# Optimization experiments

Measured on AMD Instinct MI355X. Metric: run time of the kernel, lower is better.

Reference implementation:

```python
import jax, jax.numpy as jnp
import numpy as np

EPS = 10.0
MAX_ITER = 50
THRESH = 1e-05
N, M, D = 8192, 8192, 32


def setup_inputs() -> dict:
    key = jax.random.key(0)
    k1, k2, k3, k4 = jax.random.split(key, 4)
    x = jax.random.normal(k1, (N, D), dtype=jnp.float32)
    y = jax.random.normal(k2, (M, D), dtype=jnp.float32)
    p = jax.random.uniform(k3, (N,), dtype=jnp.float32)
    q = jax.random.uniform(k4, (M,), dtype=jnp.float32)
    p = p / jnp.sum(p)  # marginals must be probability vectors
    q = q / jnp.sum(q)
    return {"x": x, "y": y, "p": p, "q": q}


def _cost_matrix_l2(x, y):
    # ||x_i - y_j||^2 via the expansion, avoiding the [N, M, D] intermediate
    x2 = jnp.sum(x * x, axis=-1)  # [N]
    y2 = jnp.sum(y * y, axis=-1)  # [M]
    C = x2[:, None] + y2[None, :] - 2.0 * (x @ y.T)  # [N, M]
    return jnp.maximum(C, 0.0)


def reference(x, y, p, q):
    C = _cost_matrix_l2(x, y)          # [N, M]
    K = jnp.exp(-C / EPS)              # [N, M]

    def step(carry, _):
        a, b, done = carry
        a_new = p / (K @ b)            # [N]
        b_new = q / (K.T @ a_new)      # [M]
        err = jnp.linalg.norm(b_new - b)
        # emulate the early break: freeze (a, b) once err < thresh was hit
        a_out = jnp.where(done, a, a_new)
        b_out = jnp.where(done, b, b_new)
        done = jnp.logical_or(done, err < THRESH)
        return (a_out, b_out, done), None

    init = (jnp.zeros_like(p), jnp.ones_like(q), jnp.array(False))
    (a, b, _), _ = jax.lax.scan(step, init, None, length=MAX_ITER)

    T = a[:, None] * K * b[None, :]    # diag(a) @ K @ diag(b)
    w_cost = jnp.sum(T * C)
    return w_cost, T
```

## Files before the change

kernel.cpp:

```cpp
#include <hip/hip_runtime.h>
#include <hip/hip_fp16.h>


#define NN 8192
#define DDIM 32
#define EPSF 10.0f
#define LOG2E 1.44269504088896340736f
#define LN2F 0.69314718055994530942f
#define KLOG2 8.0f
#define THRESH2 1e-10f

#define OFF_KS   0ull
#define OFF_PART (67108864ull)
#define OFF_A    (OFF_PART + 8388608ull)
#define OFF_B    (OFF_A + 32768ull)
#define OFF_X2   (OFF_B + 32768ull)
#define OFF_Y2   (OFF_X2 + 32768ull)
#define OFF_ERR  (OFF_Y2 + 32768ull)
#define WS_NEEDED (OFF_ERR + 4096ull)

typedef float floatx2 __attribute__((ext_vector_type(2)));

#if __has_builtin(__builtin_amdgcn_cvt_pk_f32_fp8) && __has_builtin(__builtin_amdgcn_cvt_pk_fp8_f32)
#define HW_FP8 1
#else
#define HW_FP8 0
#include <hip/hip_fp8.h>
#endif

__device__ __forceinline__ void fp8x4_to_f32(unsigned int w, float* f) {
#if HW_FP8
    floatx2 lo = __builtin_amdgcn_cvt_pk_f32_fp8((int)w, false);
    floatx2 hi = __builtin_amdgcn_cvt_pk_f32_fp8((int)w, true);
    f[0] = lo.x; f[1] = lo.y; f[2] = hi.x; f[3] = hi.y;
#else
    for (int i = 0; i < 4; ++i) {
        __hip_fp8_e4m3 h; h.__x = (__hip_fp8_storage_t)((w >> (8 * i)) & 0xff);
        f[i] = (float)h;
    }
#endif
}

__device__ __forceinline__ unsigned char f32_to_fp8(float v) {
#if HW_FP8
    return (unsigned char)(__builtin_amdgcn_cvt_pk_fp8_f32(v, v, 0, false) & 0xff);
#else
    __hip_fp8_e4m3 h(v);
    return (unsigned char)h.__x;
#endif
}

__global__ __launch_bounds__(256) void k_init(const float* __restrict__ x,
                                              const float* __restrict__ y,
                                              float* __restrict__ x2,
                                              float* __restrict__ y2,
                                              float* __restrict__ b,
                                              float* __restrict__ err,
                                              float* __restrict__ out) {
    int t = blockIdx.x * 256 + threadIdx.x;
    const float4* x4 = (const float4*)(x + (size_t)t * DDIM);
    float s = 0.f;
#pragma unroll
    for (int k = 0; k < 8; ++k) { float4 v = x4[k]; s += v.x*v.x + v.y*v.y + v.z*v.z + v.w*v.w; }
    x2[t] = s;
    const float4* y4 = (const float4*)(y + (size_t)t * DDIM);
    s = 0.f;
#pragma unroll
    for (int k = 0; k < 8; ++k) { float4 v = y4[k]; s += v.x*v.x + v.y*v.y + v.z*v.z + v.w*v.w; }
    y2[t] = s;
    b[t] = 1.0f;
    if (t < 2) err[t] = 1e30f;
    if (t == 0) out[0] = 0.f;
}

__global__ __launch_bounds__(256) void k_build(const float* __restrict__ x,
                                               const float* __restrict__ y,
                                               const float* __restrict__ x2,
                                               const float* __restrict__ y2,
                                               unsigned char* __restrict__ Ks) {
    __shared__ float yT[DDIM][256];
    __shared__ float xT[DDIM][32];
    __shared__ __align__(16) unsigned char hb8[32][256];
    const int t = threadIdx.x;
    const int jb = blockIdx.x & 31;
    const int ib = blockIdx.x >> 5;
    const int colbase = jb * 256, rowbase = ib * 32;

    {
        const float4* yp = (const float4*)(y + (size_t)(colbase + t) * DDIM);
#pragma unroll
        for (int k = 0; k < 8; ++k) {
            float4 v = yp[k];
            yT[4*k+0][t] = v.x; yT[4*k+1][t] = v.y; yT[4*k+2][t] = v.z; yT[4*k+3][t] = v.w;
        }
    }
    {
        int r = t >> 3, ds = (t & 7) * 4;
        float4 v = *(const float4*)(x + (size_t)(rowbase + r) * DDIM + ds);
        xT[ds+0][r] = v.x; xT[ds+1][r] = v.y; xT[ds+2][r] = v.z; xT[ds+3][r] = v.w;
    }
    __syncthreads();

    float acc[32];
#pragma unroll
    for (int r = 0; r < 32; ++r) acc[r] = 0.f;
    for (int d = 0; d < DDIM; ++d) {
        float yv = yT[d][t];
#pragma unroll
        for (int r4 = 0; r4 < 8; ++r4) {
            float4 xv = *(const float4*)&xT[d][r4 * 4];
            acc[r4*4+0] = fmaf(xv.x, yv, acc[r4*4+0]);
            acc[r4*4+1] = fmaf(xv.y, yv, acc[r4*4+1]);
            acc[r4*4+2] = fmaf(xv.z, yv, acc[r4*4+2]);
            acc[r4*4+3] = fmaf(xv.w, yv, acc[r4*4+3]);
        }
    }
    const float y2c = y2[colbase + t];
#pragma unroll
    for (int r = 0; r < 32; ++r) {
        float Cv = fmaxf(x2[rowbase + r] + y2c - 2.f * acc[r], 0.f);
        float arg = KLOG2 - Cv * (LOG2E / EPSF);
        hb8[r][t] = f32_to_fp8(__builtin_amdgcn_exp2f(arg));
    }
    __syncthreads();
    {
        int row = t >> 3, off = (t & 7) * 32;
        uint4 v0 = *(const uint4*)&hb8[row][off];
        uint4 v1 = *(const uint4*)&hb8[row][off + 16];
        unsigned char* dst = Ks + (size_t)(rowbase + row) * NN + colbase + off;
        *(uint4*)dst = v0;
        *(uint4*)(dst + 16) = v1;
    }
}

#if HW_FP8
#define ROWFMA(KV, KC) { \
    const unsigned int* kw_ = (const unsigned int*)&(KV); \
    _Pragma("unroll") \
    for (int j4 = 0; j4 < 4; ++j4) { \
        floatx2 lo_ = __builtin_amdgcn_cvt_pk_f32_fp8((int)kw_[j4], false); \
        floatx2 hi_ = __builtin_amdgcn_cvt_pk_f32_fp8((int)kw_[j4], true); \
        const floatx2* bp_ = (const floatx2*)(b4 + ((KC) * 4 + j4) * 64 + lane); \
        rs2a += lo_ * bp_[0]; \
        rs2b += hi_ * bp_[1]; \
    } }
#define COLFMA(KV, AV) { \
    floatx2 av2_; av2_.x = (AV); av2_.y = (AV); \
    floatx2 l0_ = __builtin_amdgcn_cvt_pk_f32_fp8((int)(KV).x, false); \
    floatx2 h0_ = __builtin_amdgcn_cvt_pk_f32_fp8((int)(KV).x, true); \
    floatx2 l1_ = __builtin_amdgcn_cvt_pk_f32_fp8((int)(KV).y, false); \
    floatx2 h1_ = __builtin_amdgcn_cvt_pk_f32_fp8((int)(KV).y, true); \
    cacc2[0] += l0_ * av2_; cacc2[1] += h0_ * av2_; \
    cacc2[2] += l1_ * av2_; cacc2[3] += h1_ * av2_; }
#else
#define ROWFMA(KV, KC) { \
    const unsigned int* kw_ = (const unsigned int*)&(KV); \
    _Pragma("unroll") \
    for (int j4 = 0; j4 < 4; ++j4) { \
        float kf_[4]; \
        fp8x4_to_f32(kw_[j4], kf_); \
        float4 bv_ = b4[((KC) * 4 + j4) * 64 + lane]; \
        rs2a.x = fmaf(kf_[0], bv_.x, rs2a.x); \
        rs2b.x = fmaf(kf_[1], bv_.y, rs2b.x); \
        rs2a.y = fmaf(kf_[2], bv_.z, rs2a.y); \
        rs2b.y = fmaf(kf_[3], bv_.w, rs2b.y); \
    } }
#define COLFMA(KV, AV) { \
    float kf_[8]; \
    fp8x4_to_f32((KV).x, kf_); \
    fp8x4_to_f32((KV).y, kf_ + 4); \
    cacc2[0].x = fmaf(kf_[0], (AV), cacc2[0].x); \
    cacc2[0].y = fmaf(kf_[1], (AV), cacc2[0].y); \
    cacc2[1].x = fmaf(kf_[2], (AV), cacc2[1].x); \
    cacc2[1].y = fmaf(kf_[3], (AV), cacc2[1].y); \
    cacc2[2].x = fmaf(kf_[4], (AV), cacc2[2].x); \
    cacc2[2].y = fmaf(kf_[5], (AV), cacc2[2].y); \
    cacc2[3].x = fmaf(kf_[6], (AV), cacc2[3].x); \
    cacc2[3].y = fmaf(kf_[7], (AV), cacc2[3].y); }
#endif

__global__ __launch_bounds__(1024) void k_iter(const unsigned char* __restrict__ Ks,
                                               const float* __restrict__ bg,
                                               const float* __restrict__ p,
                                               float* __restrict__ a_out,
                                               float* __restrict__ part,
                                               float* __restrict__ err, int it) {
    __shared__ float bsw[NN];
    __shared__ float rowhalf[2][8][2];
    const int t = threadIdx.x;
    const int w = t >> 6, lane = t & 63;
    const int band = blockIdx.x * 32;
    const int rl = w >> 1, half = w & 1;

    float4 g0 = ((const float4*)bg)[2 * t];
    float4 g1 = ((const float4*)bg)[2 * t + 1];
    const uint4* kp0 = (const uint4*)(Ks + (size_t)(band + rl) * NN + half * 4096);
    uint4 ka0 = kp0[lane], ka1 = kp0[64 + lane], ka2 = kp0[128 + lane], ka3 = kp0[192 + lane];
    float ev = err[(it ^ 1) & 1];
    if (blockIdx.x == 0 && t == 0) err[it & 1] = 0.f;
    __builtin_amdgcn_sched_barrier(0);
    if (ev < THRESH2) return;

    {
        float vals[8] = {g0.x, g0.y, g0.z, g0.w, g1.x, g1.y, g1.z, g1.w};
        int c0 = t * 8;
#pragma unroll
        for (int u = 0; u < 8; ++u) {
            int c = c0 + u;
            bsw[(c >> 10) * 1024 + ((c >> 2) & 3) * 256 + ((c >> 4) & 63) * 4 + (c & 3)] = vals[u];
        }
    }
    __syncthreads();

    floatx2 cacc2[4];
    cacc2[0] = floatx2{0.f, 0.f}; cacc2[1] = floatx2{0.f, 0.f};
    cacc2[2] = floatx2{0.f, 0.f}; cacc2[3] = floatx2{0.f, 0.f};
    const float4* b4 = (const float4*)bsw;

#pragma unroll
    for (int sub = 0; sub < 4; ++sub) {
        const int sb = sub & 1;
        const uint2* kp2 = (const uint2*)(Ks + (size_t)(band + sub * 8) * NN);
        uint2 cv0 = kp2[0 * (NN / 8) + t], cv1 = kp2[1 * (NN / 8) + t],
              cv2 = kp2[2 * (NN / 8) + t], cv3 = kp2[3 * (NN / 8) + t],
              cv4 = kp2[4 * (NN / 8) + t], cv5 = kp2[5 * (NN / 8) + t],
              cv6 = kp2[6 * (NN / 8) + t], cv7 = kp2[7 * (NN / 8) + t];
        uint4 kb0 = {0,0,0,0}, kb1 = {0,0,0,0}, kb2 = {0,0,0,0}, kb3 = {0,0,0,0};
        if (sub < 3) {
            const uint4* kp = (const uint4*)(Ks + (size_t)(band + (sub + 1) * 8 + rl) * NN + half * 4096);
            kb0 = kp[lane]; kb1 = kp[64 + lane]; kb2 = kp[128 + lane]; kb3 = kp[192 + lane];
        }
        __builtin_amdgcn_sched_barrier(0);

        floatx2 rs2a = floatx2{0.f, 0.f}, rs2b = floatx2{0.f, 0.f};
        ROWFMA(ka0, half * 4 + 0)
        ROWFMA(ka1, half * 4 + 1)
        ROWFMA(ka2, half * 4 + 2)
        ROWFMA(ka3, half * 4 + 3)
        float rs = (rs2a.x + rs2a.y) + (rs2b.x + rs2b.y);
#pragma unroll
        for (int off = 32; off > 0; off >>= 1) rs += __shfl_down(rs, off, 64);
        if (lane == 0) rowhalf[sb][rl][half] = rs;
        __syncthreads();

        const int rg = band + sub * 8;
        float av0 = p[rg + 0] * __builtin_amdgcn_rcpf(rowhalf[sb][0][0] + rowhalf[sb][0][1]);
        float av1 = p[rg + 1] * __builtin_amdgcn_rcpf(rowhalf[sb][1][0] + rowhalf[sb][1][1]);
        float av2 = p[rg + 2] * __builtin_amdgcn_rcpf(rowhalf[sb][2][0] + rowhalf[sb][2][1]);
        float av3 = p[rg + 3] * __builtin_amdgcn_rcpf(rowhalf[sb][3][0] + rowhalf[sb][3][1]);
        float av4 = p[rg + 4] * __builtin_amdgcn_rcpf(rowhalf[sb][4][0] + rowhalf[sb][4][1]);
        float av5 = p[rg + 5] * __builtin_amdgcn_rcpf(rowhalf[sb][5][0] + rowhalf[sb][5][1]);
        float av6 = p[rg + 6] * __builtin_amdgcn_rcpf(rowhalf[sb][6][0] + rowhalf[sb][6][1]);
        float av7 = p[rg + 7] * __builtin_amdgcn_rcpf(rowhalf[sb][7][0] + rowhalf[sb][7][1]);
        if (t == 0) {
            *(float4*)(a_out + rg)     = make_float4(av0, av1, av2, av3);
            *(float4*)(a_out + rg + 4) = make_float4(av4, av5, av6, av7);
        }

        COLFMA(cv0, av0)
        COLFMA(cv1, av1)
        COLFMA(cv2, av2)
        COLFMA(cv3, av3)
        COLFMA(cv4, av4)
        COLFMA(cv5, av5)
        COLFMA(cv6, av6)
        COLFMA(cv7, av7)

        if (sub < 3) { ka0 = kb0; ka1 = kb1; ka2 = kb2; ka3 = kb3; }
    }
    float4* pp = (float4*)(part + (size_t)blockIdx.x * NN + t * 8);
    pp[0] = make_float4(cacc2[0].x, cacc2[0].y, cacc2[1].x, cacc2[1].y);
    pp[1] = make_float4(cacc2[2].x, cacc2[2].y, cacc2[3].x, cacc2[3].y);
}

__global__ __launch_bounds__(256) void k_div(const float* __restrict__ part,
                                             const float* __restrict__ q,
                                             float* __restrict__ b,
                                             float* __restrict__ err, int it) {
    if (err[(it ^ 1) & 1] < THRESH2) return;
    const int t = threadIdx.x;
    const int c = t & 31, ibc = t >> 5;
    const int col = blockIdx.x * 32 + c;
    float s = 0.f;
#pragma unroll 4
    for (int i = 0; i < 32; ++i) s += part[(size_t)(ibc * 32 + i) * NN + col];
    __shared__ float red[8][32];
    __shared__ float esc[32];
    red[ibc][c] = s;
    __syncthreads();
    if (ibc == 0) {
        float sum = 0.f;
#pragma unroll
        for (int k = 0; k < 8; ++k) sum += red[k][c];
        float bn = q[col] / sum;
        float d = bn - b[col];
        b[col] = bn;
        esc[c] = d * d;
    }
    __syncthreads();
    if (t == 0) {
        float e = 0.f;
#pragma unroll
        for (int k = 0; k < 32; ++k) e += esc[k];
        atomicAdd(&err[it & 1], e);
    }
}

__global__ __launch_bounds__(256) void k_final(const unsigned char* __restrict__ Ks,
                                               const float* __restrict__ a,
                                               const float* __restrict__ b,
                                               float* __restrict__ out) {
    const int t = threadIdx.x;
    const int row = blockIdx.x;
    const float ai = a[row];
    const uint2* kp = (const uint2*)(Ks + (size_t)row * NN);
    float* Trow = out + 1 + (size_t)row * NN;
    float w = 0.f;
    const float c1 = EPSF * LN2F;
#pragma unroll
    for (int k = 0; k < 4; ++k) {
        const int col = k * 2048 + t * 8;
        uint2 kv = kp[k * 256 + t];
        float kf[8];
        fp8x4_to_f32(kv.x, kf);
        fp8x4_to_f32(kv.y, kf + 4);
        float4 b0 = *(const float4*)(b + col);
        float4 b1 = *(const float4*)(b + col + 4);
        float bv[8] = {b0.x, b0.y, b0.z, b0.w, b1.x, b1.y, b1.z, b1.w};
#pragma unroll
        for (int j = 0; j < 8; ++j) {
            float ks = kf[j];
            float Tv = ai * ks * bv[j];
            float Cv = c1 * (KLOG2 - __builtin_amdgcn_logf(fmaxf(ks, 1e-35f)));
            w = fmaf(Tv, Cv, w);
            Trow[col + j] = Tv;
        }
    }
#pragma unroll
    for (int off = 32; off > 0; off >>= 1) w += __shfl_down(w, off, 64);
    __shared__ float red[4];
    if ((t & 63) == 0) red[t >> 6] = w;
    __syncthreads();
    if (t == 0) atomicAdd(out, (red[0] + red[1]) + (red[2] + red[3]));
}

extern "C" void kernel_launch(void* const* d_in, const int* in_sizes, int n_in,
                              void* d_out, int out_size, void* d_ws, size_t ws_size,
                              hipStream_t stream) {
    const float* x = (const float*)d_in[0];
    const float* y = (const float*)d_in[1];
    const float* p = (const float*)d_in[2];
    const float* q = (const float*)d_in[3];
    float* out = (float*)d_out;
    if (ws_size < WS_NEEDED) return;
    char* ws = (char*)d_ws;
    unsigned char* Ks = (unsigned char*)(ws + OFF_KS);
    float* part = (float*)(ws + OFF_PART);
    float* a = (float*)(ws + OFF_A);
    float* b = (float*)(ws + OFF_B);
    float* x2 = (float*)(ws + OFF_X2);
    float* y2 = (float*)(ws + OFF_Y2);
    float* err = (float*)(ws + OFF_ERR);

    k_init<<<dim3(32), dim3(256), 0, stream>>>(x, y, x2, y2, b, err, out);
    k_build<<<dim3(8192), dim3(256), 0, stream>>>(x, y, x2, y2, Ks);
    for (int it = 0; it < 50; ++it) {
        k_iter<<<dim3(256), dim3(1024), 0, stream>>>(Ks, b, p, a, part, err, it);
        k_div<<<dim3(256), dim3(256), 0, stream>>>(part, q, b, err, it);
    }
    k_final<<<dim3(8192), dim3(256), 0, stream>>>(Ks, a, b, out);
}
```

Measured before the change: 1.792 ms.

## Fuse Sinkhorn iterations into one cooperative persistent kernel with grid barriers

```diff
diff --git a/kernel.cpp b/kernel.cpp
--- a/kernel.cpp
+++ b/kernel.cpp
@@ -9,6 +9,7 @@
 #define LN2F 0.69314718055994530942f
 #define KLOG2 8.0f
 #define THRESH2 1e-10f
+#define GRIDN 256
 
 #define OFF_KS   0ull
 #define OFF_PART (67108864ull)
@@ -17,6 +18,7 @@
 #define OFF_X2   (OFF_B + 32768ull)
 #define OFF_Y2   (OFF_X2 + 32768ull)
 #define OFF_ERR  (OFF_Y2 + 32768ull)
+#define OFF_BAR  (OFF_ERR + 256ull)
 #define WS_NEEDED (OFF_ERR + 4096ull)
 
 typedef float floatx2 __attribute__((ext_vector_type(2)));
@@ -50,12 +52,32 @@
 #endif
 }
 
+__device__ __forceinline__ void gsync(int* bar) {
+    __syncthreads();
+    if (threadIdx.x == 0) {
+        __threadfence();
+        int g = __hip_atomic_load(bar + 1, __ATOMIC_RELAXED, __HIP_MEMORY_SCOPE_AGENT);
+        if (__hip_atomic_fetch_add(bar, 1, __ATOMIC_ACQ_REL, __HIP_MEMORY_SCOPE_AGENT) == GRIDN - 1) {
+            __hip_atomic_store(bar, 0, __ATOMIC_RELAXED, __HIP_MEMORY_SCOPE_AGENT);
+            __hip_atomic_store(bar + 1, g + 1, __ATOMIC_RELEASE, __HIP_MEMORY_SCOPE_AGENT);
+        } else {
+            int guard = 1 << 20;
+            while (__hip_atomic_load(bar + 1, __ATOMIC_RELAXED, __HIP_MEMORY_SCOPE_AGENT) == g
+                   && --guard)
+                __builtin_amdgcn_s_sleep(2);
+        }
+        __threadfence();
+    }
+    __syncthreads();
+}
+
 __global__ __launch_bounds__(256) void k_init(const float* __restrict__ x,
                                               const float* __restrict__ y,
                                               float* __restrict__ x2,
                                               float* __restrict__ y2,
                                               float* __restrict__ b,
                                               float* __restrict__ err,
+                                              int* __restrict__ bar,
                                               float* __restrict__ out) {
     int t = blockIdx.x * 256 + threadIdx.x;
     const float4* x4 = (const float4*)(x + (size_t)t * DDIM);
@@ -69,7 +91,7 @@
     for (int k = 0; k < 8; ++k) { float4 v = y4[k]; s += v.x*v.x + v.y*v.y + v.z*v.z + v.w*v.w; }
     y2[t] = s;
     b[t] = 1.0f;
-    if (t < 2) err[t] = 1e30f;
+    if (t < 2) { err[t] = 1e30f; bar[t] = 0; }
     if (t == 0) out[0] = 0.f;
 }
 
@@ -179,6 +201,149 @@
     cacc2[3].y = fmaf(kf_[7], (AV), cacc2[3].y); }
 #endif
 
+__device__ __forceinline__ void phaseA(const unsigned char* __restrict__ Ks,
+                                       const float* __restrict__ bg,
+                                       const float* __restrict__ p,
+                                       float* __restrict__ a_out,
+                                       float* __restrict__ part,
+                                       float* bsw, float (*rowhalf)[8][2],
+                                       int t, int w, int lane, int band,
+                                       int rl, int half) {
+    float4 g0 = ((const float4*)bg)[2 * t];
+    float4 g1 = ((const float4*)bg)[2 * t + 1];
+    const uint4* kp0 = (const uint4*)(Ks + (size_t)(band + rl) * NN + half * 4096);
+    uint4 ka0 = kp0[lane], ka1 = kp0[64 + lane], ka2 = kp0[128 + lane], ka3 = kp0[192 + lane];
+    __builtin_amdgcn_sched_barrier(0);
+    {
+        float vals[8] = {g0.x, g0.y, g0.z, g0.w, g1.x, g1.y, g1.z, g1.w};
+        int c0 = t * 8;
+#pragma unroll
+        for (int u = 0; u < 8; ++u) {
+            int c = c0 + u;
+            bsw[(c >> 10) * 1024 + ((c >> 2) & 3) * 256 + ((c >> 4) & 63) * 4 + (c & 3)] = vals[u];
+        }
+    }
+    __syncthreads();
+
+    floatx2 cacc2[4];
+    cacc2[0] = floatx2{0.f, 0.f}; cacc2[1] = floatx2{0.f, 0.f};
+    cacc2[2] = floatx2{0.f, 0.f}; cacc2[3] = floatx2{0.f, 0.f};
+    const float4* b4 = (const float4*)bsw;
+
+#pragma unroll
+    for (int sub = 0; sub < 4; ++sub) {
+        const int sb = sub & 1;
+        const uint2* kp2 = (const uint2*)(Ks + (size_t)(band + sub * 8) * NN);
+        uint2 cv0 = kp2[0 * (NN / 8) + t], cv1 = kp2[1 * (NN / 8) + t],
+              cv2 = kp2[2 * (NN / 8) + t], cv3 = kp2[3 * (NN / 8) + t],
+              cv4 = kp2[4 * (NN / 8) + t], cv5 = kp2[5 * (NN / 8) + t],
+              cv6 = kp2[6 * (NN / 8) + t], cv7 = kp2[7 * (NN / 8) + t];
+        uint4 kb0 = {0,0,0,0}, kb1 = {0,0,0,0}, kb2 = {0,0,0,0}, kb3 = {0,0,0,0};
+        if (sub < 3) {
+            const uint4* kp = (const uint4*)(Ks + (size_t)(band + (sub + 1) * 8 + rl) * NN + half * 4096);
+            kb0 = kp[lane]; kb1 = kp[64 + lane]; kb2 = kp[128 + lane]; kb3 = kp[192 + lane];
+        }
+        __builtin_amdgcn_sched_barrier(0);
+
+        floatx2 rs2a = floatx2{0.f, 0.f}, rs2b = floatx2{0.f, 0.f};
+        ROWFMA(ka0, half * 4 + 0)
+        ROWFMA(ka1, half * 4 + 1)
+        ROWFMA(ka2, half * 4 + 2)
+        ROWFMA(ka3, half * 4 + 3)
+        float rs = (rs2a.x + rs2a.y) + (rs2b.x + rs2b.y);
+#pragma unroll
+        for (int off = 32; off > 0; off >>= 1) rs += __shfl_down(rs, off, 64);
+        if (lane == 0) rowhalf[sb][rl][half] = rs;
+        __syncthreads();
+
+        const int rg = band + sub * 8;
+        float av0 = p[rg + 0] * __builtin_amdgcn_rcpf(rowhalf[sb][0][0] + rowhalf[sb][0][1]);
+        float av1 = p[rg + 1] * __builtin_amdgcn_rcpf(rowhalf[sb][1][0] + rowhalf[sb][1][1]);
+        float av2 = p[rg + 2] * __builtin_amdgcn_rcpf(rowhalf[sb][2][0] + rowhalf[sb][2][1]);
+        float av3 = p[rg + 3] * __builtin_amdgcn_rcpf(rowhalf[sb][3][0] + rowhalf[sb][3][1]);
+        float av4 = p[rg + 4] * __builtin_amdgcn_rcpf(rowhalf[sb][4][0] + rowhalf[sb][4][1]);
+        float av5 = p[rg + 5] * __builtin_amdgcn_rcpf(rowhalf[sb][5][0] + rowhalf[sb][5][1]);
+        float av6 = p[rg + 6] * __builtin_amdgcn_rcpf(rowhalf[sb][6][0] + rowhalf[sb][6][1]);
+        float av7 = p[rg + 7] * __builtin_amdgcn_rcpf(rowhalf[sb][7][0] + rowhalf[sb][7][1]);
+        if (t == 0) {
+            *(float4*)(a_out + rg)     = make_float4(av0, av1, av2, av3);
+            *(float4*)(a_out + rg + 4) = make_float4(av4, av5, av6, av7);
+        }
+
+        COLFMA(cv0, av0)
+        COLFMA(cv1, av1)
+        COLFMA(cv2, av2)
+        COLFMA(cv3, av3)
+        COLFMA(cv4, av4)
+        COLFMA(cv5, av5)
+        COLFMA(cv6, av6)
+        COLFMA(cv7, av7)
+
+        if (sub < 3) { ka0 = kb0; ka1 = kb1; ka2 = kb2; ka3 = kb3; }
+    }
+    float4* pp = (float4*)(part + (size_t)blockIdx.x * NN + t * 8);
+    pp[0] = make_float4(cacc2[0].x, cacc2[0].y, cacc2[1].x, cacc2[1].y);
+    pp[1] = make_float4(cacc2[2].x, cacc2[2].y, cacc2[3].x, cacc2[3].y);
+}
+
+__global__ __launch_bounds__(1024) void k_loop(const unsigned char* __restrict__ Ks,
+                                               float* __restrict__ bg,
+                                               const float* __restrict__ p,
+                                               const float* __restrict__ q,
+                                               float* __restrict__ a_out,
+                                               float* __restrict__ part,
+                                               float* __restrict__ err,
+                                               int* __restrict__ bar) {
+    __shared__ float bsw[NN];
+    __shared__ float rowhalf[2][8][2];
+    __shared__ float redB[32][32];
+    __shared__ float esc[32];
+    const int t = threadIdx.x;
+    const int w = t >> 6, lane = t & 63;
+    const int band = blockIdx.x * 32;
+    const int rl = w >> 1, half = w & 1;
+    const int cB = t & 31, ibcB = t >> 5;
+    const int colB = blockIdx.x * 32 + cB;
+
+    for (int it = 0; it < 50; ++it) {
+        float ev = __hip_atomic_load(&err[(it ^ 1) & 1], __ATOMIC_RELAXED, __HIP_MEMORY_SCOPE_AGENT);
+        if (ev < THRESH2) break;
+        if (blockIdx.x == 0 && t == 0)
+            __hip_atomic_store(&err[it & 1], 0.f, __ATOMIC_RELAXED, __HIP_MEMORY_SCOPE_AGENT);
+
+        phaseA(Ks, bg, p, a_out, part, bsw, rowhalf, t, w, lane, band, rl, half);
+
+        gsync(bar);
+
+        {
+            float s = 0.f;
+#pragma unroll
+            for (int i = 0; i < 8; ++i) s += part[(size_t)(ibcB * 8 + i) * NN + colB];
+            redB[ibcB][cB] = s;
+            __syncthreads();
+            if (t < 32) {
+                float sum = 0.f;
+#pragma unroll
+                for (int k2 = 0; k2 < 32; ++k2) sum += redB[k2][t];
+                const int col = blockIdx.x * 32 + t;
+                float bn = q[col] / sum;
+                float d = bn - bg[col];
+                bg[col] = bn;
+                esc[t] = d * d;
+            }
+            __syncthreads();
+            if (t == 0) {
+                float e = 0.f;
+#pragma unroll
+                for (int k2 = 0; k2 < 32; ++k2) e += esc[k2];
+                atomicAdd(&err[it & 1], e);
+            }
+        }
+
+        gsync(bar);
+    }
+}
+
 __global__ __launch_bounds__(1024) void k_iter(const unsigned char* __restrict__ Ks,
                                                const float* __restrict__ bg,
                                                const float* __restrict__ p,
@@ -191,86 +356,10 @@
     const int w = t >> 6, lane = t & 63;
     const int band = blockIdx.x * 32;
     const int rl = w >> 1, half = w & 1;
-
-    float4 g0 = ((const float4*)bg)[2 * t];
-    float4 g1 = ((const float4*)bg)[2 * t + 1];
-    const uint4* kp0 = (const uint4*)(Ks + (size_t)(band + rl) * NN + half * 4096);
-    uint4 ka0 = kp0[lane], ka1 = kp0[64 + lane], ka2 = kp0[128 + lane], ka3 = kp0[192 + lane];
     float ev = err[(it ^ 1) & 1];
     if (blockIdx.x == 0 && t == 0) err[it & 1] = 0.f;
-    __builtin_amdgcn_sched_barrier(0);
     if (ev < THRESH2) return;
-
-    {
-        float vals[8] = {g0.x, g0.y, g0.z, g0.w, g1.x, g1.y, g1.z, g1.w};
-        int c0 = t * 8;
-#pragma unroll
-        for (int u = 0; u < 8; ++u) {
-            int c = c0 + u;
-            bsw[(c >> 10) * 1024 + ((c >> 2) & 3) * 256 + ((c >> 4) & 63) * 4 + (c & 3)] = vals[u];
-        }
-    }
-    __syncthreads();
-
-    floatx2 cacc2[4];
-    cacc2[0] = floatx2{0.f, 0.f}; cacc2[1] = floatx2{0.f, 0.f};
-    cacc2[2] = floatx2{0.f, 0.f}; cacc2[3] = floatx2{0.f, 0.f};
-    const float4* b4 = (const float4*)bsw;
-
-#pragma unroll
-    for (int sub = 0; sub < 4; ++sub) {
-        const int sb = sub & 1;
-        const uint2* kp2 = (const uint2*)(Ks + (size_t)(band + sub * 8) * NN);
-        uint2 cv0 = kp2[0 * (NN / 8) + t], cv1 = kp2[1 * (NN / 8) + t],
-              cv2 = kp2[2 * (NN / 8) + t], cv3 = kp2[3 * (NN / 8) + t],
-              cv4 = kp2[4 * (NN / 8) + t], cv5 = kp2[5 * (NN / 8) + t],
-              cv6 = kp2[6 * (NN / 8) + t], cv7 = kp2[7 * (NN / 8) + t];
-        uint4 kb0 = {0,0,0,0}, kb1 = {0,0,0,0}, kb2 = {0,0,0,0}, kb3 = {0,0,0,0};
-        if (sub < 3) {
-            const uint4* kp = (const uint4*)(Ks + (size_t)(band + (sub + 1) * 8 + rl) * NN + half * 4096);
-            kb0 = kp[lane]; kb1 = kp[64 + lane]; kb2 = kp[128 + lane]; kb3 = kp[192 + lane];
-        }
-        __builtin_amdgcn_sched_barrier(0);
-
-        floatx2 rs2a = floatx2{0.f, 0.f}, rs2b = floatx2{0.f, 0.f};
-        ROWFMA(ka0, half * 4 + 0)
-        ROWFMA(ka1, half * 4 + 1)
-        ROWFMA(ka2, half * 4 + 2)
-        ROWFMA(ka3, half * 4 + 3)
-        float rs = (rs2a.x + rs2a.y) + (rs2b.x + rs2b.y);
-#pragma unroll
-        for (int off = 32; off > 0; off >>= 1) rs += __shfl_down(rs, off, 64);
-        if (lane == 0) rowhalf[sb][rl][half] = rs;
-        __syncthreads();
-
-        const int rg = band + sub * 8;
-        float av0 = p[rg + 0] * __builtin_amdgcn_rcpf(rowhalf[sb][0][0] + rowhalf[sb][0][1]);
-        float av1 = p[rg + 1] * __builtin_amdgcn_rcpf(rowhalf[sb][1][0] + rowhalf[sb][1][1]);
-        float av2 = p[rg + 2] * __builtin_amdgcn_rcpf(rowhalf[sb][2][0] + rowhalf[sb][2][1]);
-        float av3 = p[rg + 3] * __builtin_amdgcn_rcpf(rowhalf[sb][3][0] + rowhalf[sb][3][1]);
-        float av4 = p[rg + 4] * __builtin_amdgcn_rcpf(rowhalf[sb][4][0] + rowhalf[sb][4][1]);
-        float av5 = p[rg + 5] * __builtin_amdgcn_rcpf(rowhalf[sb][5][0] + rowhalf[sb][5][1]);
-        float av6 = p[rg + 6] * __builtin_amdgcn_rcpf(rowhalf[sb][6][0] + rowhalf[sb][6][1]);
-        float av7 = p[rg + 7] * __builtin_amdgcn_rcpf(rowhalf[sb][7][0] + rowhalf[sb][7][1]);
-        if (t == 0) {
-            *(float4*)(a_out + rg)     = make_float4(av0, av1, av2, av3);
-            *(float4*)(a_out + rg + 4) = make_float4(av4, av5, av6, av7);
-        }
-
-        COLFMA(cv0, av0)
-        COLFMA(cv1, av1)
-        COLFMA(cv2, av2)
-        COLFMA(cv3, av3)
-        COLFMA(cv4, av4)
-        COLFMA(cv5, av5)
-        COLFMA(cv6, av6)
-        COLFMA(cv7, av7)
-
-        if (sub < 3) { ka0 = kb0; ka1 = kb1; ka2 = kb2; ka3 = kb3; }
-    }
-    float4* pp = (float4*)(part + (size_t)blockIdx.x * NN + t * 8);
-    pp[0] = make_float4(cacc2[0].x, cacc2[0].y, cacc2[1].x, cacc2[1].y);
-    pp[1] = make_float4(cacc2[2].x, cacc2[2].y, cacc2[3].x, cacc2[3].y);
+    phaseA(Ks, bg, p, a_out, part, bsw, rowhalf, t, w, lane, band, rl, half);
 }
 
 __global__ __launch_bounds__(256) void k_div(const float* __restrict__ part,
@@ -361,12 +450,21 @@
     float* x2 = (float*)(ws + OFF_X2);
     float* y2 = (float*)(ws + OFF_Y2);
     float* err = (float*)(ws + OFF_ERR);
-
-    k_init<<<dim3(32), dim3(256), 0, stream>>>(x, y, x2, y2, b, err, out);
+    int* bar = (int*)(ws + OFF_BAR);
+
+    k_init<<<dim3(32), dim3(256), 0, stream>>>(x, y, x2, y2, b, err, bar, out);
     k_build<<<dim3(8192), dim3(256), 0, stream>>>(x, y, x2, y2, Ks);
-    for (int it = 0; it < 50; ++it) {
-        k_iter<<<dim3(256), dim3(1024), 0, stream>>>(Ks, b, p, a, part, err, it);
-        k_div<<<dim3(256), dim3(256), 0, stream>>>(part, q, b, err, it);
+
+    void* args[] = { (void*)&Ks, (void*)&b, (void*)&p, (void*)&q,
+                     (void*)&a, (void*)&part, (void*)&err, (void*)&bar };
+    hipError_t ce = hipLaunchCooperativeKernel((void*)k_loop, dim3(GRIDN), dim3(1024),
+                                               args, 0, stream);
+    if (ce != hipSuccess) {
+        (void)hipGetLastError();
+        for (int it = 0; it < 50; ++it) {
+            k_iter<<<dim3(GRIDN), dim3(1024), 0, stream>>>(Ks, b, p, a, part, err, it);
+            k_div<<<dim3(256), dim3(256), 0, stream>>>(part, q, b, err, it);
+        }
     }
     k_final<<<dim3(8192), dim3(256), 0, stream>>>(Ks, a, b, out);
 }
```

Result: slower. 5.161 ms (+187.9%).
